# Performance work log

Hardware: AMD Instinct MI355X
Metric: run time of the kernel (lower is better)

Reference implementation:

```python
import jax, jax.numpy as jnp
import numpy as np

NUM_ATOMS = 512
NUM_DIMS = 128
H = 32
W = 32
B = 32


def make_dct_dict():
    # rows i: cos((2n+1) * i * pi / (2*num_dims)), L2-normalized; Dict = weights.T -> [D, A]
    i = jnp.arange(NUM_ATOMS, dtype=jnp.float32)[:, None]
    n = jnp.arange(NUM_DIMS, dtype=jnp.float32)[None, :]
    atoms = jnp.cos((2.0 * n + 1.0) * i * (np.pi / (2.0 * NUM_DIMS)))  # [A, D]
    atoms = atoms / jnp.linalg.norm(atoms, axis=1, keepdims=True)
    return atoms.T  # [D, A]


def setup_inputs() -> dict:
    key = jax.random.key(0)
    x = jax.random.normal(key, (B, NUM_DIMS, H, W), dtype=jnp.float32)
    Dict = make_dct_dict()                      # [D, A] learned param (DCT init)
    L = jnp.sum(Dict ** 2)                      # ||Dict||_F^2 (scalar param)
    alpha = jnp.ones((1, H, W, 1), dtype=jnp.float32)  # learned threshold param
    return {"x": x, "Dict": Dict, "alpha": alpha, "L": L, "num_iters": 16}


def reference(x, Dict, alpha, L, num_iters):
    l = alpha / L                                # [1,H,W,1] threshold, broadcasts over atoms
    xt = jnp.transpose(x, (0, 2, 3, 1))          # [B,H,W,D]
    S = (jnp.eye(NUM_ATOMS, dtype=Dict.dtype) - (Dict.T @ Dict) / L).T  # [A,A]
    y = xt @ Dict                                # [B,H,W,A]

    def soft_thresh(v):
        return jnp.sign(v) * jnp.maximum(jnp.abs(v) - l, 0.0)

    z = soft_thresh(y)

    def body(z, _):
        z = soft_thresh(z @ S + y / L)
        return z, None

    z, _ = jax.lax.scan(body, z, None, length=num_iters)
    x_recon = z @ Dict.T                         # [B,H,W,D]
    return (jnp.transpose(z, (0, 3, 1, 2)),      # [B,A,H,W]
            jnp.transpose(x_recon, (0, 3, 1, 2)),  # [B,D,H,W]
            Dict)
```

## Files before the change

kernel.cpp:

```cpp
#include <hip/hip_runtime.h>
#include <hip/hip_bf16.h>

typedef __bf16 bf16_t;
typedef bf16_t bf16x8 __attribute__((ext_vector_type(8)));
typedef float f32x4 __attribute__((ext_vector_type(4)));
typedef unsigned short u16;
typedef unsigned int u32;

static __device__ __forceinline__ u16 f2bf(float f) {
    __hip_bfloat16 h = __float2bfloat16(f);
    return __builtin_bit_cast(u16, h);
}
static __device__ __forceinline__ bf16_t fb(float f) {
    return __builtin_bit_cast(bf16_t, f2bf(f));
}
static __device__ __forceinline__ float bf2f(u16 u) {
    u32 x = ((u32)u) << 16;
    return __builtin_bit_cast(float, x);
}
static __device__ __forceinline__ float softthr(float v, float l) {
    return copysignf(fmaxf(fabsf(v) - l, 0.0f), v);
}

__global__ __launch_bounds__(256) void copy_dict(const float* __restrict__ Dict,
                                                 float* __restrict__ outd)
{
    int i = blockIdx.x * 256 + threadIdx.x;
    outd[i] = Dict[i];
}

__global__ __launch_bounds__(512, 2)
void lista_main(const float* __restrict__ x,
                const float* __restrict__ Dict,
                const float* __restrict__ alpha,
                const float* __restrict__ Lp,
                const int* __restrict__ nip,
                float* __restrict__ outz,
                float* __restrict__ outr)
{
    __shared__ __align__(16) u16 zl[2][16 * 512];
    __shared__ __align__(16) u16 rl[2][16 * 128];
    __shared__ __align__(16) u16 xs[2][16 * 128];
    __shared__ __align__(16) u16 pb[2][16 * 4 * 128];

    const int t = threadIdx.x;
    const int lane = t & 63;
    const int l15 = lane & 15;
    const int lg = lane >> 4;
    const int wave = t >> 6;
    const int dg = wave >> 2;
    const int ag = wave & 3;
    const int atb = wave << 6;
    const int bb = blockIdx.x >> 5;
    const int hw0 = (blockIdx.x & 31) << 5;
    const float invL = 1.0f / Lp[0];
    const int niter = nip[0];

    for (int i = t; i < 2 * 16 * 128; i += 512) {
        int tt = i >> 11, j = i & 2047;
        int d = j >> 4, px = j & 15;
        xs[tt][((px << 7) + d) ^ ((px & 7) << 3)] =
            f2bf(x[((bb * 128 + d) << 10) + hw0 + tt * 16 + px]);
    }

    const float thrA = alpha[hw0 + l15] * invL;
    const float thrB = alpha[hw0 + 16 + l15] * invL;

    bf16x8 g1a[4][4];
#pragma unroll
    for (int mt = 0; mt < 4; ++mt) {
        const float* drow = Dict + ((dg * 64 + mt * 16 + l15) << 9) + ag * 128 + lg * 8;
#pragma unroll
        for (int kt = 0; kt < 4; ++kt) {
            f32x4 c0 = *reinterpret_cast<const f32x4*>(drow + kt * 32);
            f32x4 c1 = *reinterpret_cast<const f32x4*>(drow + kt * 32 + 4);
#pragma unroll
            for (int j = 0; j < 4; ++j) {
                g1a[mt][kt][j] = fb(-c0[j]);
                g1a[mt][kt][j + 4] = fb(-c1[j]);
            }
        }
    }
    bf16x8 g2a[4][4];
#pragma unroll
    for (int at = 0; at < 4; ++at)
#pragma unroll
        for (int kt = 0; kt < 4; ++kt)
#pragma unroll
            for (int j = 0; j < 8; ++j)
                g2a[at][kt][j] = fb(Dict[((kt * 32 + lg * 8 + j) << 9) + atb + at * 16 + l15]);

    __syncthreads();

    auto g2_tile = [&](f32x4 (&acc)[4], u16* __restrict__ zlt,
                       const u16* __restrict__ bsrc, float thv) {
#pragma unroll
        for (int kt = 0; kt < 4; ++kt) {
            const int px = l15;
            bf16x8 Bf = *reinterpret_cast<const bf16x8*>(
                &bsrc[((px << 7) + kt * 32 + lg * 8) ^ ((px & 7) << 3)]);
            __builtin_amdgcn_s_setprio(1);
#pragma unroll
            for (int at = 0; at < 4; ++at)
                acc[at] = __builtin_amdgcn_mfma_f32_16x16x32_bf16(
                    g2a[at][kt], Bf, acc[at], 0, 0, 0);
            __builtin_amdgcn_s_setprio(0);
        }
#pragma unroll
        for (int at = 0; at < 4; ++at) {
            const int px = l15;
            f32x4 a = acc[at];
            a[0] = softthr(a[0], thv);
            a[1] = softthr(a[1], thv);
            a[2] = softthr(a[2], thv);
            a[3] = softthr(a[3], thv);
            acc[at] = a;
            uint2 pk;
            pk.x = (u32)f2bf(a[0]) | ((u32)f2bf(a[1]) << 16);
            pk.y = (u32)f2bf(a[2]) | ((u32)f2bf(a[3]) << 16);
            *reinterpret_cast<uint2*>(
                &zlt[((px << 9) + atb + at * 16 + lg * 4) ^ ((px & 7) << 3)]) = pk;
        }
    };

    auto g1_tile = [&](const u16* __restrict__ zlt, u16* __restrict__ pbt) {
        f32x4 a1p[4];
#pragma unroll
        for (int mt = 0; mt < 4; ++mt)
            a1p[mt] = f32x4{0.f, 0.f, 0.f, 0.f};
#pragma unroll
        for (int kt = 0; kt < 4; ++kt) {
            const int px = l15;
            bf16x8 Bf = *reinterpret_cast<const bf16x8*>(
                &zlt[((px << 9) + ag * 128 + kt * 32 + lg * 8) ^ ((px & 7) << 3)]);
            __builtin_amdgcn_s_setprio(1);
#pragma unroll
            for (int mt = 0; mt < 4; ++mt)
                a1p[mt] = __builtin_amdgcn_mfma_f32_16x16x32_bf16(
                    g1a[mt][kt], Bf, a1p[mt], 0, 0, 0);
            __builtin_amdgcn_s_setprio(0);
        }
#pragma unroll
        for (int mt = 0; mt < 4; ++mt) {
            const int px = l15;
            int d0 = dg * 64 + mt * 16 + lg * 4;
            f32x4 a = a1p[mt];
            uint2 pk;
            pk.x = (u32)f2bf(a[0]) | ((u32)f2bf(a[1]) << 16);
            pk.y = (u32)f2bf(a[2]) | ((u32)f2bf(a[3]) << 16);
            *reinterpret_cast<uint2*>(
                &pbt[((px << 9) + (ag << 7) + d0) ^ ((px & 7) << 3)]) = pk;
        }
    };

    auto reduce_all = [&]() {
        const int tt = t >> 8;
        const int px = (t >> 4) & 15;
        const int roc = t & 15;
        const u16* pbt = &pb[0][0] + (tt << 13);
        const u16* xst = &xs[0][0] + (tt << 11);
        u16* rlt = &rl[0][0] + (tt << 11);
        const int sw = (px & 7) << 3;
        bf16x8 p0 = *reinterpret_cast<const bf16x8*>(&pbt[((px << 9) + 0 * 128 + roc * 8) ^ sw]);
        bf16x8 p1 = *reinterpret_cast<const bf16x8*>(&pbt[((px << 9) + 1 * 128 + roc * 8) ^ sw]);
        bf16x8 p2 = *reinterpret_cast<const bf16x8*>(&pbt[((px << 9) + 2 * 128 + roc * 8) ^ sw]);
        bf16x8 p3 = *reinterpret_cast<const bf16x8*>(&pbt[((px << 9) + 3 * 128 + roc * 8) ^ sw]);
        bf16x8 xv = *reinterpret_cast<const bf16x8*>(&xst[((px << 7) + roc * 8) ^ sw]);
        bf16x8 rv;
#pragma unroll
        for (int e = 0; e < 8; ++e) {
            float s = ((float)xv[e] + (float)p0[e]) + ((float)p1[e] + (float)p2[e]) + (float)p3[e];
            rv[e] = fb(s * invL);
        }
        *reinterpret_cast<bf16x8*>(&rlt[((px << 7) + roc * 8) ^ sw]) = rv;
    };

    f32x4 acczA[4], acczB[4];
#pragma unroll
    for (int at = 0; at < 4; ++at) {
        acczA[at] = f32x4{0.f, 0.f, 0.f, 0.f};
        acczB[at] = f32x4{0.f, 0.f, 0.f, 0.f};
    }

    g2_tile(acczA, zl[0], xs[0], thrA);
    g2_tile(acczB, zl[1], xs[1], thrB);
    __syncthreads();

    for (int it = 1; it <= niter; ++it) {
        g1_tile(zl[0], pb[0]);
        g1_tile(zl[1], pb[1]);
        __syncthreads();
        reduce_all();
        __syncthreads();
        g2_tile(acczA, zl[0], rl[0], thrA);
        g2_tile(acczB, zl[1], rl[1], thrB);
        __syncthreads();
    }

    g1_tile(zl[0], pb[0]);
    g1_tile(zl[1], pb[1]);
    __syncthreads();

    float rec[8];
    {
        const int tt = t >> 8;
        const int px = (t >> 4) & 15;
        const int roc = t & 15;
        const u16* pbt = &pb[0][0] + (tt << 13);
        const int sw = (px & 7) << 3;
        bf16x8 p0 = *reinterpret_cast<const bf16x8*>(&pbt[((px << 9) + 0 * 128 + roc * 8) ^ sw]);
        bf16x8 p1 = *reinterpret_cast<const bf16x8*>(&pbt[((px << 9) + 1 * 128 + roc * 8) ^ sw]);
        bf16x8 p2 = *reinterpret_cast<const bf16x8*>(&pbt[((px << 9) + 2 * 128 + roc * 8) ^ sw]);
        bf16x8 p3 = *reinterpret_cast<const bf16x8*>(&pbt[((px << 9) + 3 * 128 + roc * 8) ^ sw]);
#pragma unroll
        for (int e = 0; e < 8; ++e)
            rec[e] = -(((float)p0[e] + (float)p1[e]) + ((float)p2[e] + (float)p3[e]));
    }

    for (int i = t; i < 2 * 16 * 512; i += 512) {
        int tt = i >> 13, j = i & 8191;
        int a = j >> 4, px = j & 15;
        float zv = bf2f(zl[tt][((px << 9) + a) ^ ((px & 7) << 3)]);
        __builtin_nontemporal_store(zv, &outz[((bb * 512 + a) << 10) + hw0 + tt * 16 + px]);
    }
    __syncthreads();

    {
        const int tt = t >> 8;
        const int px = (t >> 4) & 15;
        const int roc = t & 15;
        float* wf = reinterpret_cast<float*>(&pb[0][0]) + (tt << 12);
        const int swf = (px & 7) << 2;
#pragma unroll
        for (int e = 0; e < 8; ++e)
            wf[((px << 7) + roc * 8 + e) ^ swf] = rec[e];
    }
    __syncthreads();

    for (int i = t; i < 2 * 16 * 128; i += 512) {
        int tt = i >> 11, j = i & 2047;
        int d = j >> 4, px = j & 15;
        const float* wf = reinterpret_cast<const float*>(&pb[0][0]) + (tt << 12);
        __builtin_nontemporal_store(wf[((px << 7) + d) ^ ((px & 7) << 2)],
                                    &outr[((bb * 128 + d) << 10) + hw0 + tt * 16 + px]);
    }
}

extern "C" void kernel_launch(void* const* d_in, const int* in_sizes, int n_in,
                              void* d_out, int out_size, void* d_ws, size_t ws_size,
                              hipStream_t stream)
{
    const float* x     = (const float*)d_in[0];
    const float* Dict  = (const float*)d_in[1];
    const float* alpha = (const float*)d_in[2];
    const float* Lp    = (const float*)d_in[3];
    const int*   nip   = (const int*)d_in[4];

    float* outz = (float*)d_out;
    float* outr = outz + 32 * 512 * 1024;
    float* outd = outr + 32 * 128 * 1024;

    copy_dict<<<dim3(256), dim3(256), 0, stream>>>(Dict, outd);
    lista_main<<<dim3(1024), dim3(512), 0, stream>>>(x, Dict, alpha, Lp, nip,
                                                     outz, outr);
}
```

Before: 209.9 us.

## Software-pipeline two pixel tiles across LISTA stages and fuse G1/G2 matmuls

Restructures the iteration loop so the two 16-pixel tiles are staggered: one tile's reduction runs while the other's D-projection MFMAs run, and a fused g1_g2 routine interleaves both matmuls in one k-loop. Each barrier phase now mixes MFMA and LDS/VALU work from different tiles instead of running lockstep phases that are purely matmul or purely reduction. It also drops the s_setprio hints, uses native packed bf16 conversions, and rewrites soft-threshold as a min/max form. The reduction is split per tile with narrower vectors. The added schedule complexity raises register pressure, which could hurt occupancy under launch_bounds(512,2).

Result: slower. 219.7 us (+4.7%).

```diff
diff --git a/kernel.cpp b/kernel.cpp
--- a/kernel.cpp
+++ b/kernel.cpp
@@ -2,24 +2,27 @@
 #include <hip/hip_bf16.h>
 
 typedef __bf16 bf16_t;
+typedef bf16_t bf16x2 __attribute__((ext_vector_type(2)));
 typedef bf16_t bf16x8 __attribute__((ext_vector_type(8)));
 typedef float f32x4 __attribute__((ext_vector_type(4)));
 typedef unsigned short u16;
 typedef unsigned int u32;
 
-static __device__ __forceinline__ u16 f2bf(float f) {
-    __hip_bfloat16 h = __float2bfloat16(f);
-    return __builtin_bit_cast(u16, h);
-}
-static __device__ __forceinline__ bf16_t fb(float f) {
-    return __builtin_bit_cast(bf16_t, f2bf(f));
+static __device__ __forceinline__ u16 cvt1(float f) {
+    return __builtin_bit_cast(u16, (bf16_t)f);
+}
+static __device__ __forceinline__ u32 cvt2(float a, float b) {
+    bf16x2 t; t[0] = (bf16_t)a; t[1] = (bf16_t)b;
+    return __builtin_bit_cast(u32, t);
 }
 static __device__ __forceinline__ float bf2f(u16 u) {
     u32 x = ((u32)u) << 16;
     return __builtin_bit_cast(float, x);
 }
-static __device__ __forceinline__ float softthr(float v, float l) {
-    return copysignf(fmaxf(fabsf(v) - l, 0.0f), v);
+static __device__ __forceinline__ float lo32(u32 p) { return __builtin_bit_cast(float, p << 16); }
+static __device__ __forceinline__ float hi32(u32 p) { return __builtin_bit_cast(float, p & 0xffff0000u); }
+static __device__ __forceinline__ float softthr(float v, float l, float nl) {
+    return v - fmaxf(nl, fminf(v, l));
 }
 
 __global__ __launch_bounds__(256) void copy_dict(const float* __restrict__ Dict,
@@ -38,10 +41,10 @@
                 float* __restrict__ outz,
                 float* __restrict__ outr)
 {
-    __shared__ __align__(16) u16 zl[2][16 * 512];
-    __shared__ __align__(16) u16 rl[2][16 * 128];
-    __shared__ __align__(16) u16 xs[2][16 * 128];
-    __shared__ __align__(16) u16 pb[2][16 * 4 * 128];
+    __shared__ __align__(16) u16 zlA[16 * 512], zlB[16 * 512];
+    __shared__ __align__(16) u16 rlA[16 * 128], rlB[16 * 128];
+    __shared__ __align__(16) u16 xsA[16 * 128], xsB[16 * 128];
+    __shared__ __align__(16) u16 pbA[16 * 512], pbB[16 * 512];
 
     const int t = threadIdx.x;
     const int lane = t & 63;
@@ -55,16 +58,18 @@
     const int hw0 = (blockIdx.x & 31) << 5;
     const float invL = 1.0f / Lp[0];
     const int niter = nip[0];
+    const int sw0 = (l15 & 7) << 3;
 
     for (int i = t; i < 2 * 16 * 128; i += 512) {
         int tt = i >> 11, j = i & 2047;
         int d = j >> 4, px = j & 15;
-        xs[tt][((px << 7) + d) ^ ((px & 7) << 3)] =
-            f2bf(x[((bb * 128 + d) << 10) + hw0 + tt * 16 + px]);
-    }
-
-    const float thrA = alpha[hw0 + l15] * invL;
-    const float thrB = alpha[hw0 + 16 + l15] * invL;
+        u16* xst = tt ? xsB : xsA;
+        xst[((px << 7) + d) ^ ((px & 7) << 3)] =
+            cvt1(x[((bb * 128 + d) << 10) + hw0 + tt * 16 + px]);
+    }
+
+    const float thrA = alpha[hw0 + l15] * invL,      nthrA = -thrA;
+    const float thrB = alpha[hw0 + 16 + l15] * invL, nthrB = -thrB;
 
     bf16x8 g1a[4][4];
 #pragma unroll
@@ -76,8 +81,8 @@
             f32x4 c1 = *reinterpret_cast<const f32x4*>(drow + kt * 32 + 4);
 #pragma unroll
             for (int j = 0; j < 4; ++j) {
-                g1a[mt][kt][j] = fb(-c0[j]);
-                g1a[mt][kt][j + 4] = fb(-c1[j]);
+                g1a[mt][kt][j] = (bf16_t)(-c0[j]);
+                g1a[mt][kt][j + 4] = (bf16_t)(-c1[j]);
             }
         }
     }
@@ -88,91 +93,126 @@
         for (int kt = 0; kt < 4; ++kt)
 #pragma unroll
             for (int j = 0; j < 8; ++j)
-                g2a[at][kt][j] = fb(Dict[((kt * 32 + lg * 8 + j) << 9) + atb + at * 16 + l15]);
-
-    __syncthreads();
-
-    auto g2_tile = [&](f32x4 (&acc)[4], u16* __restrict__ zlt,
-                       const u16* __restrict__ bsrc, float thv) {
+                g2a[at][kt][j] = (bf16_t)(Dict[((kt * 32 + lg * 8 + j) << 9) + atb + at * 16 + l15]);
+
+    __syncthreads();
+
+    auto g2_tile = [&](f32x4 (&acc)[4], u16* zlt, const u16* bsrc,
+                       float thv, float nthv) {
 #pragma unroll
         for (int kt = 0; kt < 4; ++kt) {
-            const int px = l15;
             bf16x8 Bf = *reinterpret_cast<const bf16x8*>(
-                &bsrc[((px << 7) + kt * 32 + lg * 8) ^ ((px & 7) << 3)]);
-            __builtin_amdgcn_s_setprio(1);
+                &bsrc[((l15 << 7) + kt * 32 + lg * 8) ^ sw0]);
 #pragma unroll
             for (int at = 0; at < 4; ++at)
                 acc[at] = __builtin_amdgcn_mfma_f32_16x16x32_bf16(
                     g2a[at][kt], Bf, acc[at], 0, 0, 0);
-            __builtin_amdgcn_s_setprio(0);
         }
 #pragma unroll
         for (int at = 0; at < 4; ++at) {
-            const int px = l15;
             f32x4 a = acc[at];
-            a[0] = softthr(a[0], thv);
-            a[1] = softthr(a[1], thv);
-            a[2] = softthr(a[2], thv);
-            a[3] = softthr(a[3], thv);
+            a[0] = softthr(a[0], thv, nthv);
+            a[1] = softthr(a[1], thv, nthv);
+            a[2] = softthr(a[2], thv, nthv);
+            a[3] = softthr(a[3], thv, nthv);
             acc[at] = a;
             uint2 pk;
-            pk.x = (u32)f2bf(a[0]) | ((u32)f2bf(a[1]) << 16);
-            pk.y = (u32)f2bf(a[2]) | ((u32)f2bf(a[3]) << 16);
+            pk.x = cvt2(a[0], a[1]);
+            pk.y = cvt2(a[2], a[3]);
             *reinterpret_cast<uint2*>(
-                &zlt[((px << 9) + atb + at * 16 + lg * 4) ^ ((px & 7) << 3)]) = pk;
+                &zlt[((l15 << 9) + atb + at * 16 + lg * 4) ^ sw0]) = pk;
         }
     };
 
-    auto g1_tile = [&](const u16* __restrict__ zlt, u16* __restrict__ pbt) {
+    auto g1_tile = [&](const u16* zlt, u16* pbt) {
         f32x4 a1p[4];
 #pragma unroll
         for (int mt = 0; mt < 4; ++mt)
             a1p[mt] = f32x4{0.f, 0.f, 0.f, 0.f};
 #pragma unroll
         for (int kt = 0; kt < 4; ++kt) {
-            const int px = l15;
             bf16x8 Bf = *reinterpret_cast<const bf16x8*>(
-                &zlt[((px << 9) + ag * 128 + kt * 32 + lg * 8) ^ ((px & 7) << 3)]);
-            __builtin_amdgcn_s_setprio(1);
+                &zlt[((l15 << 9) + ag * 128 + kt * 32 + lg * 8) ^ sw0]);
 #pragma unroll
             for (int mt = 0; mt < 4; ++mt)
                 a1p[mt] = __builtin_amdgcn_mfma_f32_16x16x32_bf16(
                     g1a[mt][kt], Bf, a1p[mt], 0, 0, 0);
-            __builtin_amdgcn_s_setprio(0);
         }
 #pragma unroll
         for (int mt = 0; mt < 4; ++mt) {
-            const int px = l15;
             int d0 = dg * 64 + mt * 16 + lg * 4;
-            f32x4 a = a1p[mt];
             uint2 pk;
-            pk.x = (u32)f2bf(a[0]) | ((u32)f2bf(a[1]) << 16);
-            pk.y = (u32)f2bf(a[2]) | ((u32)f2bf(a[3]) << 16);
+            pk.x = cvt2(a1p[mt][0], a1p[mt][1]);
+            pk.y = cvt2(a1p[mt][2], a1p[mt][3]);
             *reinterpret_cast<uint2*>(
-                &pbt[((px << 9) + (ag << 7) + d0) ^ ((px & 7) << 3)]) = pk;
+                &pbt[((l15 << 9) + (ag << 7) + d0) ^ sw0]) = pk;
         }
     };
 
-    auto reduce_all = [&]() {
-        const int tt = t >> 8;
-        const int px = (t >> 4) & 15;
-        const int roc = t & 15;
-        const u16* pbt = &pb[0][0] + (tt << 13);
-        const u16* xst = &xs[0][0] + (tt << 11);
-        u16* rlt = &rl[0][0] + (tt << 11);
+    auto g1_g2 = [&](const u16* zl_r, u16* pb_w,
+                     f32x4 (&acc)[4], u16* zl_w, const u16* bsrc,
+                     float thv, float nthv) {
+        f32x4 a1p[4];
+#pragma unroll
+        for (int mt = 0; mt < 4; ++mt)
+            a1p[mt] = f32x4{0.f, 0.f, 0.f, 0.f};
+#pragma unroll
+        for (int kt = 0; kt < 4; ++kt) {
+            bf16x8 Bf1 = *reinterpret_cast<const bf16x8*>(
+                &zl_r[((l15 << 9) + ag * 128 + kt * 32 + lg * 8) ^ sw0]);
+            bf16x8 Bf2 = *reinterpret_cast<const bf16x8*>(
+                &bsrc[((l15 << 7) + kt * 32 + lg * 8) ^ sw0]);
+#pragma unroll
+            for (int mt = 0; mt < 4; ++mt)
+                a1p[mt] = __builtin_amdgcn_mfma_f32_16x16x32_bf16(
+                    g1a[mt][kt], Bf1, a1p[mt], 0, 0, 0);
+#pragma unroll
+            for (int at = 0; at < 4; ++at)
+                acc[at] = __builtin_amdgcn_mfma_f32_16x16x32_bf16(
+                    g2a[at][kt], Bf2, acc[at], 0, 0, 0);
+        }
+#pragma unroll
+        for (int mt = 0; mt < 4; ++mt) {
+            int d0 = dg * 64 + mt * 16 + lg * 4;
+            uint2 pk;
+            pk.x = cvt2(a1p[mt][0], a1p[mt][1]);
+            pk.y = cvt2(a1p[mt][2], a1p[mt][3]);
+            *reinterpret_cast<uint2*>(
+                &pb_w[((l15 << 9) + (ag << 7) + d0) ^ sw0]) = pk;
+        }
+#pragma unroll
+        for (int at = 0; at < 4; ++at) {
+            f32x4 a = acc[at];
+            a[0] = softthr(a[0], thv, nthv);
+            a[1] = softthr(a[1], thv, nthv);
+            a[2] = softthr(a[2], thv, nthv);
+            a[3] = softthr(a[3], thv, nthv);
+            acc[at] = a;
+            uint2 pk;
+            pk.x = cvt2(a[0], a[1]);
+            pk.y = cvt2(a[2], a[3]);
+            *reinterpret_cast<uint2*>(
+                &zl_w[((l15 << 9) + atb + at * 16 + lg * 4) ^ sw0]) = pk;
+        }
+    };
+
+    auto reduce_tile = [&](const u16* pbt, const u16* xst, u16* rlt) {
+        const int px = t >> 5;
+        const int d0 = (t & 31) << 2;
         const int sw = (px & 7) << 3;
-        bf16x8 p0 = *reinterpret_cast<const bf16x8*>(&pbt[((px << 9) + 0 * 128 + roc * 8) ^ sw]);
-        bf16x8 p1 = *reinterpret_cast<const bf16x8*>(&pbt[((px << 9) + 1 * 128 + roc * 8) ^ sw]);
-        bf16x8 p2 = *reinterpret_cast<const bf16x8*>(&pbt[((px << 9) + 2 * 128 + roc * 8) ^ sw]);
-        bf16x8 p3 = *reinterpret_cast<const bf16x8*>(&pbt[((px << 9) + 3 * 128 + roc * 8) ^ sw]);
-        bf16x8 xv = *reinterpret_cast<const bf16x8*>(&xst[((px << 7) + roc * 8) ^ sw]);
-        bf16x8 rv;
-#pragma unroll
-        for (int e = 0; e < 8; ++e) {
-            float s = ((float)xv[e] + (float)p0[e]) + ((float)p1[e] + (float)p2[e]) + (float)p3[e];
-            rv[e] = fb(s * invL);
-        }
-        *reinterpret_cast<bf16x8*>(&rlt[((px << 7) + roc * 8) ^ sw]) = rv;
+        uint2 P0 = *reinterpret_cast<const uint2*>(&pbt[((px << 9) + 0 * 128 + d0) ^ sw]);
+        uint2 P1 = *reinterpret_cast<const uint2*>(&pbt[((px << 9) + 1 * 128 + d0) ^ sw]);
+        uint2 P2 = *reinterpret_cast<const uint2*>(&pbt[((px << 9) + 2 * 128 + d0) ^ sw]);
+        uint2 P3 = *reinterpret_cast<const uint2*>(&pbt[((px << 9) + 3 * 128 + d0) ^ sw]);
+        uint2 XV = *reinterpret_cast<const uint2*>(&xst[((px << 7) + d0) ^ sw]);
+        float s0 = (lo32(XV.x) + lo32(P0.x)) + (lo32(P1.x) + lo32(P2.x)) + lo32(P3.x);
+        float s1 = (hi32(XV.x) + hi32(P0.x)) + (hi32(P1.x) + hi32(P2.x)) + hi32(P3.x);
+        float s2 = (lo32(XV.y) + lo32(P0.y)) + (lo32(P1.y) + lo32(P2.y)) + lo32(P3.y);
+        float s3 = (hi32(XV.y) + hi32(P0.y)) + (hi32(P1.y) + hi32(P2.y)) + hi32(P3.y);
+        uint2 rv;
+        rv.x = cvt2(s0 * invL, s1 * invL);
+        rv.y = cvt2(s2 * invL, s3 * invL);
+        *reinterpret_cast<uint2*>(&rlt[((px << 7) + d0) ^ sw]) = rv;
     };
 
     f32x4 acczA[4], acczB[4];
@@ -182,65 +222,80 @@
         acczB[at] = f32x4{0.f, 0.f, 0.f, 0.f};
     }
 
-    g2_tile(acczA, zl[0], xs[0], thrA);
-    g2_tile(acczB, zl[1], xs[1], thrB);
-    __syncthreads();
-
-    for (int it = 1; it <= niter; ++it) {
-        g1_tile(zl[0], pb[0]);
-        g1_tile(zl[1], pb[1]);
+    g2_tile(acczA, zlA, xsA, thrA, nthrA);
+    __syncthreads();
+    g1_g2(zlA, pbA, acczB, zlB, xsB, thrB, nthrB);
+    __syncthreads();
+
+    for (int k = 1; k <= niter; ++k) {
+        reduce_tile(pbA, xsA, rlA);
+        g1_tile(zlB, pbB);
         __syncthreads();
-        reduce_all();
+        g2_tile(acczA, zlA, rlA, thrA, nthrA);
+        reduce_tile(pbB, xsB, rlB);
         __syncthreads();
-        g2_tile(acczA, zl[0], rl[0], thrA);
-        g2_tile(acczB, zl[1], rl[1], thrB);
+        g1_g2(zlA, pbA, acczB, zlB, rlB, thrB, nthrB);
         __syncthreads();
     }
 
-    g1_tile(zl[0], pb[0]);
-    g1_tile(zl[1], pb[1]);
-    __syncthreads();
-
-    float rec[8];
+    float recA[4];
     {
-        const int tt = t >> 8;
-        const int px = (t >> 4) & 15;
-        const int roc = t & 15;
-        const u16* pbt = &pb[0][0] + (tt << 13);
+        const int px = t >> 5;
+        const int d0 = (t & 31) << 2;
         const int sw = (px & 7) << 3;
-        bf16x8 p0 = *reinterpret_cast<const bf16x8*>(&pbt[((px << 9) + 0 * 128 + roc * 8) ^ sw]);
-        bf16x8 p1 = *reinterpret_cast<const bf16x8*>(&pbt[((px << 9) + 1 * 128 + roc * 8) ^ sw]);
-        bf16x8 p2 = *reinterpret_cast<const bf16x8*>(&pbt[((px << 9) + 2 * 128 + roc * 8) ^ sw]);
-        bf16x8 p3 = *reinterpret_cast<const bf16x8*>(&pbt[((px << 9) + 3 * 128 + roc * 8) ^ sw]);
-#pragma unroll
-        for (int e = 0; e < 8; ++e)
-            rec[e] = -(((float)p0[e] + (float)p1[e]) + ((float)p2[e] + (float)p3[e]));
+        uint2 P0 = *reinterpret_cast<const uint2*>(&pbA[((px << 9) + 0 * 128 + d0) ^ sw]);
+        uint2 P1 = *reinterpret_cast<const uint2*>(&pbA[((px << 9) + 1 * 128 + d0) ^ sw]);
+        uint2 P2 = *reinterpret_cast<const uint2*>(&pbA[((px << 9) + 2 * 128 + d0) ^ sw]);
+        uint2 P3 = *reinterpret_cast<const uint2*>(&pbA[((px << 9) + 3 * 128 + d0) ^ sw]);
+        recA[0] = -((lo32(P0.x) + lo32(P1.x)) + (lo32(P2.x) + lo32(P3.x)));
+        recA[1] = -((hi32(P0.x) + hi32(P1.x)) + (hi32(P2.x) + hi32(P3.x)));
+        recA[2] = -((lo32(P0.y) + lo32(P1.y)) + (lo32(P2.y) + lo32(P3.y)));
+        recA[3] = -((hi32(P0.y) + hi32(P1.y)) + (hi32(P2.y) + hi32(P3.y)));
+    }
+    g1_tile(zlB, pbB);
+    __syncthreads();
+
+    float recB[4];
+    {
+        const int px = t >> 5;
+        const int d0 = (t & 31) << 2;
+        const int sw = (px & 7) << 3;
+        uint2 P0 = *reinterpret_cast<const uint2*>(&pbB[((px << 9) + 0 * 128 + d0) ^ sw]);
+        uint2 P1 = *reinterpret_cast<const uint2*>(&pbB[((px << 9) + 1 * 128 + d0) ^ sw]);
+        uint2 P2 = *reinterpret_cast<const uint2*>(&pbB[((px << 9) + 2 * 128 + d0) ^ sw]);
+        uint2 P3 = *reinterpret_cast<const uint2*>(&pbB[((px << 9) + 3 * 128 + d0) ^ sw]);
+        recB[0] = -((lo32(P0.x) + lo32(P1.x)) + (lo32(P2.x) + lo32(P3.x)));
+        recB[1] = -((hi32(P0.x) + hi32(P1.x)) + (hi32(P2.x) + hi32(P3.x)));
+        recB[2] = -((lo32(P0.y) + lo32(P1.y)) + (lo32(P2.y) + lo32(P3.y)));
+        recB[3] = -((hi32(P0.y) + hi32(P1.y)) + (hi32(P2.y) + hi32(P3.y)));
     }
 
     for (int i = t; i < 2 * 16 * 512; i += 512) {
         int tt = i >> 13, j = i & 8191;
         int a = j >> 4, px = j & 15;
-        float zv = bf2f(zl[tt][((px << 9) + a) ^ ((px & 7) << 3)]);
+        const u16* zlt = tt ? zlB : zlA;
+        float zv = bf2f(zlt[((px << 9) + a) ^ ((px & 7) << 3)]);
         __builtin_nontemporal_store(zv, &outz[((bb * 512 + a) << 10) + hw0 + tt * 16 + px]);
     }
     __syncthreads();
 
     {
-        const int tt = t >> 8;
-        const int px = (t >> 4) & 15;
-        const int roc = t & 15;
-        float* wf = reinterpret_cast<float*>(&pb[0][0]) + (tt << 12);
+        const int px = t >> 5;
+        const int d0 = (t & 31) << 2;
         const int swf = (px & 7) << 2;
-#pragma unroll
-        for (int e = 0; e < 8; ++e)
-            wf[((px << 7) + roc * 8 + e) ^ swf] = rec[e];
+        float* wfA = reinterpret_cast<float*>(pbA);
+        float* wfB = reinterpret_cast<float*>(pbB);
+        f32x4 va{recA[0], recA[1], recA[2], recA[3]};
+        f32x4 vb{recB[0], recB[1], recB[2], recB[3]};
+        *reinterpret_cast<f32x4*>(&wfA[((px << 7) + d0) ^ swf]) = va;
+        *reinterpret_cast<f32x4*>(&wfB[((px << 7) + d0) ^ swf]) = vb;
     }
     __syncthreads();
 
     for (int i = t; i < 2 * 16 * 128; i += 512) {
         int tt = i >> 11, j = i & 2047;
         int d = j >> 4, px = j & 15;
-        const float* wf = reinterpret_cast<const float*>(&pb[0][0]) + (tt << 12);
+        const float* wf = reinterpret_cast<const float*>(tt ? pbB : pbA);
         __builtin_nontemporal_store(wf[((px << 7) + d) ^ ((px & 7) << 2)],
                                     &outr[((bb * 128 + d) << 10) + hw0 + tt * 16 + px]);
     }
```
